# Kernel optimization log

Measured on AMD Instinct MI355X. Metric: run time of the kernel, lower is better.

The kernel has to match this reference:

```python
import jax, jax.numpy as jnp
import numpy as np

NUM_GROUPS = 32
EPS = 1e-6


def group_norm(x, gamma, beta):
    # x: [b, c, h, w]
    b, c, h, w = x.shape
    g = NUM_GROUPS
    xg = x.reshape(b, g, c // g, h, w)
    mean = jnp.mean(xg, axis=(2, 3, 4), keepdims=True)
    var = jnp.var(xg, axis=(2, 3, 4), keepdims=True)
    xg = (xg - mean) * jax.lax.rsqrt(var + EPS)
    x = xg.reshape(b, c, h, w)
    return x * gamma[None, :, None, None] + beta[None, :, None, None]


def conv1x1(x, w, bias):
    # x: [b, c_in, h, w], w: [c_out, c_in], bias: [c_out]
    return jnp.einsum('bihw,oi->bohw', x, w) + bias[None, :, None, None]


def setup_inputs() -> dict:
    key = jax.random.key(0)
    ks = jax.random.split(key, 10)
    c = 512
    b, h, w = 4, 64, 64
    scale = 1.0 / np.sqrt(c)
    inp = {
        'x': jax.random.normal(ks[0], (b, c, h, w), dtype=jnp.float32),
        'gn_gamma': jnp.ones((c,), dtype=jnp.float32),
        'gn_beta': jnp.zeros((c,), dtype=jnp.float32),
        'wq': jax.random.normal(ks[1], (c, c), dtype=jnp.float32) * scale,
        'bq': jnp.zeros((c,), dtype=jnp.float32),
        'wk': jax.random.normal(ks[2], (c, c), dtype=jnp.float32) * scale,
        'bk': jnp.zeros((c,), dtype=jnp.float32),
        'wv': jax.random.normal(ks[3], (c, c), dtype=jnp.float32) * scale,
        'bv': jnp.zeros((c,), dtype=jnp.float32),
        'wo': jax.random.normal(ks[4], (c, c), dtype=jnp.float32) * scale,
        'bo': jnp.zeros((c,), dtype=jnp.float32),
    }
    return inp


def reference(x, gn_gamma, gn_beta, wq, bq, wk, bk, wv, bv, wo, bo):
    b, c, h, w = x.shape
    h_ = group_norm(x, gn_gamma, gn_beta)
    q = conv1x1(h_, wq, bq)
    k = conv1x1(h_, wk, bk)
    v = conv1x1(h_, wv, bv)
    n = h * w
    q = q.reshape(b, c, n).transpose(0, 2, 1)  # [b, n, c]
    k = k.reshape(b, c, n)                      # [b, c, n]
    v = v.reshape(b, c, n).transpose(0, 2, 1)  # [b, n, c]
    sim = jnp.einsum('bqc,bck->bqk', q, k) * (c ** -0.5)  # [b, n, n]
    attn = jax.nn.softmax(sim, axis=-1)
    out = jnp.einsum('bqk,bkc->bqc', attn, v)  # [b, n, c]
    out = out.transpose(0, 2, 1).reshape(b, c, h, w)
    out = conv1x1(out, wo, bo)
    return x + out
```

## Files before the change

kernel.cpp:

```cpp
#include <hip/hip_runtime.h>


typedef __attribute__((ext_vector_type(8))) short bf16x8;
typedef __attribute__((ext_vector_type(4))) float f32x4;

#define MFMA16(a, b, c) __builtin_amdgcn_mfma_f32_16x16x32_bf16((a), (b), (c), 0, 0, 0)

#define B_   4
#define C_   512
#define N_   4096
#define SCALE 0.044194173824159216f
#define ESHIFT 12.0f
#define SC2   0.06376297465050853f
#define ES2   17.312340490667562f

__device__ __forceinline__ unsigned short f2bf(float f) {
    union { float f; unsigned int u; } v; v.f = f;
    unsigned int r = (v.u + 0x7fffu + ((v.u >> 16) & 1u)) >> 16;
    return (unsigned short)r;
}
__device__ __forceinline__ float bf2f(unsigned short s) {
    union { unsigned int u; float f; } v; v.u = ((unsigned int)s) << 16;
    return v.f;
}

__device__ __forceinline__ void async16(const unsigned short* g, unsigned short* l) {
    __builtin_amdgcn_global_load_lds((const __attribute__((address_space(1))) unsigned int*)g,
                                     (__attribute__((address_space(3))) unsigned int*)l,
                                     16, 0, 0);
}

__global__ __launch_bounds__(256) void gn_partial(const float* __restrict__ x,
                                                  float* __restrict__ part) {
    int blk = blockIdx.x;
    int gid = blk >> 2, qtr = blk & 3;
    const float4* base = (const float4*)(x + (size_t)gid * 65536) + qtr * 4096;
    float s = 0.f, ss = 0.f;
    for (int i = threadIdx.x; i < 4096; i += 256) {
        float4 v = base[i];
        s  += v.x + v.y + v.z + v.w;
        ss += v.x * v.x + v.y * v.y + v.z * v.z + v.w * v.w;
    }
    __shared__ float red[512];
    int t = threadIdx.x;
    red[t] = s; red[256 + t] = ss;
    __syncthreads();
    for (int st = 128; st > 0; st >>= 1) {
        if (t < st) { red[t] += red[t + st]; red[256 + t] += red[256 + t + st]; }
        __syncthreads();
    }
    if (t == 0) { part[blk] = red[0]; part[512 + blk] = red[256]; }
}

__global__ __launch_bounds__(256) void gn_apply(const float* __restrict__ x,
                                                const float* __restrict__ gamma,
                                                const float* __restrict__ beta,
                                                const float* __restrict__ part,
                                                unsigned short* __restrict__ ht) {
    __shared__ float tile[64][65];
    __shared__ float mrs[4][2];
    int j0 = blockIdx.x * 64, c0 = blockIdx.y * 64, b = blockIdx.z;
    int t = threadIdx.x;
    if (t < 4) {
        int gid = b * 32 + (c0 >> 4) + t;
        float s = 0.f, ss = 0.f;
#pragma unroll
        for (int q = 0; q < 4; ++q) { s += part[gid * 4 + q]; ss += part[512 + gid * 4 + q]; }
        float mean = s * (1.f / 65536.f);
        float var  = ss * (1.f / 65536.f) - mean * mean;
        mrs[t][0] = mean;
        mrs[t][1] = rsqrtf(var + 1e-6f);
    }
    __syncthreads();
#pragma unroll
    for (int i = 0; i < 16; ++i) {
        int lid = i * 256 + t;
        int cl = lid >> 6, jl = lid & 63;
        int c = c0 + cl;
        float v = x[((size_t)b * C_ + c) * N_ + j0 + jl];
        tile[cl][jl] = (v - mrs[cl >> 4][0]) * mrs[cl >> 4][1] * gamma[c] + beta[c];
    }
    __syncthreads();
#pragma unroll
    for (int i = 0; i < 16; ++i) {
        int lid = i * 256 + t;
        int jl = lid >> 6, cl = lid & 63;
        ht[((size_t)b * N_ + j0 + jl) * C_ + c0 + cl] = f2bf(tile[cl][jl]);
    }
}

__global__ __launch_bounds__(256) void wconv(const float* __restrict__ wq,
                                             const float* __restrict__ wk,
                                             const float* __restrict__ wv,
                                             const float* __restrict__ wo,
                                             unsigned short* __restrict__ dst) {
    size_t i = (size_t)blockIdx.x * 256 + threadIdx.x;
    int m = (int)(i >> 18);
    size_t off = i & 262143;
    const float* src = (m == 0) ? wq : (m == 1) ? wk : (m == 2) ? wv : wo;
    dst[i] = f2bf(src[off]);
}

template <typename EPI>
__device__ __forceinline__ void gemm_core(const unsigned short* __restrict__ Abase,
                                          const unsigned short* __restrict__ Bbase,
                                          size_t lda, size_t ldb, int K, EPI epi) {
    __shared__ unsigned short hl[2][128 * 64];
    __shared__ unsigned short wl[2][128 * 64];
    int t = threadIdx.x;
    int wv = t >> 6, lane = t & 63, l15 = lane & 15, quad = lane >> 4;
    int wm = wv & 1, wn = wv >> 1;
    int srow = lane >> 3;
    int sch  = ((lane & 7) ^ srow) * 8;
    int xr = l15 & 7;
    f32x4 acc[4][4] = {};
#pragma unroll
    for (int i = 0; i < 4; ++i) {
        int seg = wv * 4 + i;
        size_t row = seg * 8 + srow;
        async16(&Abase[row * lda + sch], &hl[0][seg * 512]);
        async16(&Bbase[row * ldb + sch], &wl[0][seg * 512]);
    }
    int nk = K >> 6;
    for (int k = 0; k < nk; ++k) {
        int cur = k & 1;
        __builtin_amdgcn_s_waitcnt(0x3F70);
        __syncthreads();
        if (k + 1 < nk) {
            int k0 = (k + 1) << 6;
#pragma unroll
            for (int i = 0; i < 4; ++i) {
                int seg = wv * 4 + i;
                size_t row = seg * 8 + srow;
                async16(&Abase[row * lda + k0 + sch], &hl[cur ^ 1][seg * 512]);
                async16(&Bbase[row * ldb + k0 + sch], &wl[cur ^ 1][seg * 512]);
            }
        }
#pragma unroll
        for (int kk = 0; kk < 2; ++kk) {
            int sl = (((kk << 2) + quad) ^ xr) * 8;
            bf16x8 af[4], bfr[4];
#pragma unroll
            for (int mi = 0; mi < 4; ++mi)
                af[mi] = *(const bf16x8*)&hl[cur][(wm * 64 + mi * 16 + l15) * 64 + sl];
#pragma unroll
            for (int ni = 0; ni < 4; ++ni)
                bfr[ni] = *(const bf16x8*)&wl[cur][(wn * 64 + ni * 16 + l15) * 64 + sl];
#pragma unroll
            for (int mi = 0; mi < 4; ++mi)
#pragma unroll
                for (int ni = 0; ni < 4; ++ni)
                    acc[mi][ni] = MFMA16(af[mi], bfr[ni], acc[mi][ni]);
        }
    }
    epi(acc, wm, wn, l15, quad);
}

__global__ __launch_bounds__(256) void gemm_qkv(const unsigned short* __restrict__ Ht,
                                                const unsigned short* __restrict__ Wb,
                                                const float* __restrict__ bq,
                                                const float* __restrict__ bk,
                                                const float* __restrict__ bv,
                                                unsigned short* __restrict__ Qt,
                                                unsigned short* __restrict__ Kt,
                                                unsigned short* __restrict__ Vg) {
    int b = blockIdx.z, j0 = blockIdx.x * 128;
    int ct = blockIdx.y;
    int slab = ct >> 2, co0 = (ct & 3) * 128;
    const unsigned short* A = Ht + ((size_t)b * N_ + j0) * C_;
    const unsigned short* B = Wb + (size_t)slab * C_ * C_ + (size_t)co0 * C_;
    const float* bias = (slab == 0) ? bq : (slab == 1) ? bk : bv;
    unsigned short* outqk = (slab == 0) ? Qt : Kt;
    gemm_core(A, B, C_, C_, C_,
        [&](f32x4 (&acc)[4][4], int wm, int wn, int l15, int quad) {
        if (slab < 2) {
#pragma unroll
            for (int mi = 0; mi < 4; ++mi)
#pragma unroll
                for (int ni = 0; ni < 4; ++ni)
#pragma unroll
                    for (int r = 0; r < 4; ++r) {
                        int mrow = wm * 64 + mi * 16 + quad * 4 + r;
                        int ncol = wn * 64 + ni * 16 + l15;
                        outqk[((size_t)b * N_ + j0 + mrow) * C_ + co0 + ncol] =
                            f2bf(acc[mi][ni][r] + bias[co0 + ncol]);
                    }
        } else {
#pragma unroll
            for (int mi = 0; mi < 4; ++mi)
#pragma unroll
                for (int ni = 0; ni < 4; ++ni) {
                    int ncol = wn * 64 + ni * 16 + l15;
                    float bb = bias[co0 + ncol];
                    ushort4 pk;
                    pk.x = f2bf(acc[mi][ni][0] + bb);
                    pk.y = f2bf(acc[mi][ni][1] + bb);
                    pk.z = f2bf(acc[mi][ni][2] + bb);
                    pk.w = f2bf(acc[mi][ni][3] + bb);
                    int jb = j0 + wm * 64 + mi * 16 + quad * 4;
                    *(ushort4*)&Vg[((size_t)b * C_ + co0 + ncol) * N_ + jb] = pk;
                }
        }
    });
}

__global__ __launch_bounds__(512, 2) void gemm_qk_exp(const unsigned short* __restrict__ Qt,
                                                      const unsigned short* __restrict__ Kt,
                                                      unsigned short* __restrict__ P,
                                                      float* __restrict__ psum) {
    extern __shared__ unsigned short sm[];
    int lin = blockIdx.x + 16 * blockIdx.y + 256 * blockIdx.z;
    int xcd = lin & 7;
    int i4  = lin >> 3;
    int idx = i4 & 31;
    int b   = i4 >> 5;
    int rq  = xcd & 3, rk = xcd >> 2;
    int j0  = (rq * 4 + (idx & 3)) * 256;
    int ky  = rk * 8 + (idx >> 2);
    int kc0 = ky * 256;
    const unsigned short* A  = Qt + ((size_t)b * N_ + j0) * C_;
    const unsigned short* Bm = Kt + ((size_t)b * N_ + kc0) * C_;

    int t = threadIdx.x;
    int w = t >> 6, lane = t & 63, l15 = lane & 15, quad = lane >> 4;
    int wm = w >> 2, wn = w & 3;
    int srow = lane >> 2;
    int sch  = (((lane & 3) ^ ((lane >> 3) & 3))) * 8;
    int slotq = (quad ^ ((l15 >> 1) & 3)) * 8;

    f32x4 acc[8][4] = {};

    const int NT = 16;
#pragma unroll
    for (int tt = 0; tt < 2; ++tt) {
        unsigned short* dst = sm + (tt << 14);
        size_t k0 = (size_t)tt << 5;
#pragma unroll
        for (int i = 0; i < 2; ++i) {
            int seg = w * 2 + i;
            size_t row = (size_t)seg * 16 + srow;
            async16(&A [row * C_ + k0 + sch], dst + seg * 512);
            async16(&Bm[row * C_ + k0 + sch], dst + 8192 + seg * 512);
        }
    }
    __builtin_amdgcn_s_waitcnt(0x3F74);
    __builtin_amdgcn_s_barrier();

    for (int tt = 0; tt < NT; tt += 2) {
#pragma unroll
        for (int s = 0; s < 2; ++s) {
            int tc = tt + s;
            const unsigned short* bp = sm + ((tc & 3) << 14);
            int ts = tc + 2;
            unsigned short* stg = sm + ((ts & 3) << 14);
            const bool dostage = (ts < NT);
            size_t k0n = (size_t)ts << 5;
            bf16x8 bfr[4], af[4], af2[4];
#pragma unroll
            for (int ni = 0; ni < 4; ++ni)
                bfr[ni] = *(const bf16x8*)&bp[8192 + (wn * 64 + ni * 16 + l15) * 32 + slotq];
#pragma unroll
            for (int mi = 0; mi < 4; ++mi)
                af[mi] = *(const bf16x8*)&bp[(wm * 128 + mi * 16 + l15) * 32 + slotq];
            if (dostage) {
#pragma unroll
                for (int i = 0; i < 2; ++i) {
                    int seg = w * 2 + i;
                    size_t row = (size_t)seg * 16 + srow;
                    async16(&A[row * C_ + k0n + sch], stg + seg * 512);
                }
            }
            __builtin_amdgcn_s_setprio(1);
#pragma unroll
            for (int mi = 0; mi < 4; ++mi)
#pragma unroll
                for (int ni = 0; ni < 4; ++ni)
                    acc[mi][ni] = MFMA16(af[mi], bfr[ni], acc[mi][ni]);
            __builtin_amdgcn_s_setprio(0);
#pragma unroll
            for (int mi = 0; mi < 4; ++mi)
                af2[mi] = *(const bf16x8*)&bp[(wm * 128 + (mi + 4) * 16 + l15) * 32 + slotq];
            if (dostage) {
#pragma unroll
                for (int i = 0; i < 2; ++i) {
                    int seg = w * 2 + i;
                    size_t row = (size_t)seg * 16 + srow;
                    async16(&Bm[row * C_ + k0n + sch], stg + 8192 + seg * 512);
                }
            }
            __builtin_amdgcn_s_setprio(1);
#pragma unroll
            for (int mi = 0; mi < 4; ++mi)
#pragma unroll
                for (int ni = 0; ni < 4; ++ni)
                    acc[4 + mi][ni] = MFMA16(af2[mi], bfr[ni], acc[4 + mi][ni]);
            __builtin_amdgcn_s_setprio(0);
            if (s == 0) {
                if (tt + 2 < NT) __builtin_amdgcn_s_waitcnt(0x3F74);
                else             __builtin_amdgcn_s_waitcnt(0x3F70);
                __builtin_amdgcn_sched_barrier(0);
            }
        }
        if (tt + 2 < NT) {
            if (tt + 3 < NT) __builtin_amdgcn_s_waitcnt(0x3F74);
            else             __builtin_amdgcn_s_waitcnt(0x3F70);
            __builtin_amdgcn_s_barrier();
        }
    }

#pragma unroll
    for (int mi = 0; mi < 8; ++mi) {
        float rs[4] = {0.f, 0.f, 0.f, 0.f};
#pragma unroll
        for (int ni = 0; ni < 4; ++ni) {
            int ncol = kc0 + wn * 64 + ni * 16 + l15;
#pragma unroll
            for (int r = 0; r < 4; ++r) {
                int mrow = j0 + wm * 128 + mi * 16 + quad * 4 + r;
                float p = exp2f(__builtin_fmaf(acc[mi][ni][r], SC2, -ES2));
                rs[r] += p;
                P[((size_t)b * N_ + mrow) * N_ + ncol] = f2bf(p);
            }
        }
#pragma unroll
        for (int r = 0; r < 4; ++r) {
            float v = rs[r];
            v += __shfl_xor(v, 1);
            v += __shfl_xor(v, 2);
            v += __shfl_xor(v, 4);
            v += __shfl_xor(v, 8);
            if (l15 == 0)
                psum[(size_t)(wn * 16 + ky) * 16384 +
                     (size_t)b * N_ + j0 + wm * 128 + mi * 16 + quad * 4 + r] = v;
        }
    }
}

__global__ __launch_bounds__(512, 2) void gemm_pv(const unsigned short* __restrict__ P,
                                                  const unsigned short* __restrict__ Vg,
                                                  const float* __restrict__ psum,
                                                  unsigned short* __restrict__ ao) {
    extern __shared__ unsigned short sm[];
    __shared__ float linv[256];
    int lin = blockIdx.x;
    int xcd = lin & 7;
    int i4  = lin >> 3;
    int ct  = i4 & 3;
    int grp = xcd + 8 * (i4 >> 2);
    int b = grp & 3, qtile = grp >> 2;
    int j0 = qtile * 256, co0 = ct * 128;
    int t = threadIdx.x;
    int w = t >> 6, lane = t & 63, l15 = lane & 15, quad = lane >> 4;
    int wm = w >> 1, wn = w & 1;
    int srow = lane >> 2;
    int sch  = ((lane & 3) ^ ((lane >> 3) & 3)) * 8;
    int slotq = (quad ^ ((l15 >> 1) & 3)) * 8;
    const unsigned short* A  = P  + ((size_t)b * N_ + j0) * N_;
    const unsigned short* Bm = Vg + ((size_t)b * C_ + co0) * N_;
    f32x4 acc[4][4] = {};
    const int NT = 128;
#pragma unroll
    for (int tt = 0; tt < 2; ++tt) {
        unsigned short* dst = sm + tt * 12288;
        size_t k0 = (size_t)tt << 5;
#pragma unroll
        for (int i = 0; i < 2; ++i) {
            int seg = w * 2 + i;
            size_t row = (size_t)seg * 16 + srow;
            async16(&A[row * N_ + k0 + sch], dst + seg * 512);
        }
        {
            size_t row = (size_t)w * 16 + srow;
            async16(&Bm[row * N_ + k0 + sch], dst + 8192 + w * 512);
        }
    }
    if (t < 256) {
        size_t q = (size_t)b * N_ + j0 + t;
        float s = 0.f;
#pragma unroll
        for (int i = 0; i < 64; ++i) s += psum[(size_t)i * 16384 + q];
        linv[t] = 1.f / s;
    }
    __builtin_amdgcn_s_waitcnt(0x3F73);
    __builtin_amdgcn_s_barrier();
    for (int tt = 0; tt < NT; tt += 2) {
#pragma unroll
        for (int s = 0; s < 2; ++s) {
            int tc = tt + s;
            const unsigned short* bp = sm + (tc & 3) * 12288;
            int ts = tc + 2;
            bf16x8 af[4], bfr[4];
#pragma unroll
            for (int mi = 0; mi < 4; ++mi)
                af[mi] = *(const bf16x8*)&bp[(wm * 64 + mi * 16 + l15) * 32 + slotq];
#pragma unroll
            for (int ni = 0; ni < 4; ++ni)
                bfr[ni] = *(const bf16x8*)&bp[8192 + (wn * 64 + ni * 16 + l15) * 32 + slotq];
            if (ts < NT) {
                unsigned short* stg = sm + (ts & 3) * 12288;
                size_t k0n = (size_t)ts << 5;
#pragma unroll
                for (int i = 0; i < 2; ++i) {
                    int seg = w * 2 + i;
                    size_t row = (size_t)seg * 16 + srow;
                    async16(&A[row * N_ + k0n + sch], stg + seg * 512);
                }
                {
                    size_t row = (size_t)w * 16 + srow;
                    async16(&Bm[row * N_ + k0n + sch], stg + 8192 + w * 512);
                }
            }
            __builtin_amdgcn_s_setprio(1);
#pragma unroll
            for (int mi = 0; mi < 4; ++mi)
#pragma unroll
                for (int ni = 0; ni < 4; ++ni)
                    acc[mi][ni] = MFMA16(af[mi], bfr[ni], acc[mi][ni]);
            __builtin_amdgcn_s_setprio(0);
            if (s == 0) {
                if (tt + 2 < NT) __builtin_amdgcn_s_waitcnt(0x3F73);
                else             __builtin_amdgcn_s_waitcnt(0x3F70);
                __builtin_amdgcn_sched_barrier(0);
            }
        }
        if (tt + 2 < NT) {
            if (tt + 3 < NT) __builtin_amdgcn_s_waitcnt(0x3F73);
            else             __builtin_amdgcn_s_waitcnt(0x3F70);
            __builtin_amdgcn_s_barrier();
        }
    }
#pragma unroll
    for (int mi = 0; mi < 4; ++mi)
#pragma unroll
        for (int ni = 0; ni < 4; ++ni)
#pragma unroll
            for (int r = 0; r < 4; ++r) {
                int mrow = wm * 64 + mi * 16 + quad * 4 + r;
                int ncol = wn * 64 + ni * 16 + l15;
                ao[((size_t)b * N_ + j0 + mrow) * C_ + co0 + ncol] =
                    f2bf(acc[mi][ni][r] * linv[mrow]);
            }
}

__global__ __launch_bounds__(256) void gemm_resid(const unsigned short* __restrict__ AObf,
                                                  const unsigned short* __restrict__ Wo,
                                                  const float* __restrict__ bo,
                                                  const float* __restrict__ xres,
                                                  float* __restrict__ out) {
    int b = blockIdx.z, j0 = blockIdx.x * 128, co0 = blockIdx.y * 128;
    const unsigned short* A = AObf + ((size_t)b * N_ + j0) * C_;
    const unsigned short* B = Wo + (size_t)co0 * C_;
    gemm_core(A, B, C_, C_, C_,
        [&](f32x4 (&acc)[4][4], int wm, int wn, int l15, int quad) {
#pragma unroll
        for (int mi = 0; mi < 4; ++mi)
#pragma unroll
            for (int ni = 0; ni < 4; ++ni) {
                int ncol = wn * 64 + ni * 16 + l15;
                int jb = j0 + wm * 64 + mi * 16 + quad * 4;
                size_t o = ((size_t)b * C_ + co0 + ncol) * N_ + jb;
                float bb = bo[co0 + ncol];
                float4 xr = *(const float4*)&xres[o];
                float4 ov;
                ov.x = acc[mi][ni][0] + bb + xr.x;
                ov.y = acc[mi][ni][1] + bb + xr.y;
                ov.z = acc[mi][ni][2] + bb + xr.z;
                ov.w = acc[mi][ni][3] + bb + xr.w;
                *(float4*)&out[o] = ov;
            }
    });
}

__global__ __launch_bounds__(256, 1) void flash_attn(const unsigned short* __restrict__ Qt,
                                                     const unsigned short* __restrict__ Kt,
                                                     const unsigned short* __restrict__ Vg,
                                                     unsigned short* __restrict__ part,
                                                     float* __restrict__ lbuf,
                                                     int nsplit) {
    extern __shared__ unsigned short smem[];
    unsigned short* Kl = smem;
    unsigned short* Vl = smem + 32768;
    unsigned short* Pl = smem + 65536;

    int flat = blockIdx.x;
    int qblk, b, s;
    if (nsplit == 2) { s = flat & 1; b = (flat >> 1) & 3; qblk = flat >> 3; }
    else             { s = 0;        b = flat & 3;        qblk = flat >> 2; }
    int q0 = qblk * 128;
    int t = threadIdx.x, w = t >> 6, lane = t & 63, l15 = lane & 15, quad = lane >> 4;
    int klen = N_ / nsplit, kbeg = s * klen, nkt = klen / 32;
    int xr = l15 & 7;

    const unsigned short* Kbase = Kt + (size_t)b * N_ * C_;
    const unsigned short* Vbase = Vg + (size_t)b * C_ * N_;

    bf16x8 qa[2][16];
#pragma unroll
    for (int u = 0; u < 2; ++u) {
        const unsigned short* qb =
            Qt + ((size_t)b * N_ + q0 + w * 32 + u * 16 + l15) * C_ + quad * 8;
#pragma unroll
        for (int ck = 0; ck < 16; ++ck) qa[u][ck] = *(const bf16x8*)(qb + ck * 32);
    }

    f32x4 o[2][32] = {};
    float lrow[2][4] = {};

    {
        int k0 = kbeg;
#pragma unroll
        for (int i = 0; i < 8; ++i) {
            int r = w * 8 + i;
            async16(Kbase + (size_t)(k0 + r) * C_ + ((lane ^ (r & 7)) * 8), Kl + r * 512);
        }
#pragma unroll
        for (int i = 0; i < 8; ++i) {
            int idx = w * 8 + i, kc = idx >> 3, cb = idx & 7;
            async16(Vbase + (size_t)(cb * 64 + lane) * N_ + k0 + kc * 8,
                    Vl + (kc * 512 + cb * 64) * 8);
        }
    }

    for (int kt = 0; kt < nkt; ++kt) {
        int cur = kt & 1, nxt = cur ^ 1;
        __builtin_amdgcn_s_waitcnt(0x3F70);
        __syncthreads();
        if (kt + 1 < nkt) {
            int k0 = kbeg + (kt + 1) * 32;
#pragma unroll
            for (int i = 0; i < 8; ++i) {
                int r = w * 8 + i;
                async16(Kbase + (size_t)(k0 + r) * C_ + ((lane ^ (r & 7)) * 8),
                        Kl + nxt * 16384 + r * 512);
            }
#pragma unroll
            for (int i = 0; i < 8; ++i) {
                int idx = w * 8 + i, kc = idx >> 3, cb = idx & 7;
                async16(Vbase + (size_t)(cb * 64 + lane) * N_ + k0 + kc * 8,
                        Vl + nxt * 16384 + (kc * 512 + cb * 64) * 8);
            }
        }
        const unsigned short* Kc = Kl + cur * 16384;
        f32x4 s00 = {}, s01 = {}, s10 = {}, s11 = {};
#pragma unroll
        for (int ck = 0; ck < 16; ++ck) {
            int slot = (ck * 4 + quad) ^ xr;
            bf16x8 b0 = *(const bf16x8*)&Kc[l15 * 512 + slot * 8];
            bf16x8 b1 = *(const bf16x8*)&Kc[(16 + l15) * 512 + slot * 8];
            s00 = MFMA16(qa[0][ck], b0, s00);
            s10 = MFMA16(qa[1][ck], b0, s10);
            s01 = MFMA16(qa[0][ck], b1, s01);
            s11 = MFMA16(qa[1][ck], b1, s11);
        }
        unsigned short* pb = &Pl[w * 1152];
#pragma unroll
        for (int r = 0; r < 4; ++r) {
            float p00 = __expf(s00[r] * SCALE - ESHIFT);
            float p01 = __expf(s01[r] * SCALE - ESHIFT);
            float p10 = __expf(s10[r] * SCALE - ESHIFT);
            float p11 = __expf(s11[r] * SCALE - ESHIFT);
            lrow[0][r] += p00 + p01;
            lrow[1][r] += p10 + p11;
            int row0 = (quad * 4 + r) * 36;
            int row1 = (16 + quad * 4 + r) * 36;
            pb[row0 + l15]      = f2bf(p00);
            pb[row0 + 16 + l15] = f2bf(p01);
            pb[row1 + l15]      = f2bf(p10);
            pb[row1 + 16 + l15] = f2bf(p11);
        }
        __builtin_amdgcn_s_waitcnt(0xC07F);
        bf16x8 pa0 = *(const bf16x8*)&Pl[w * 1152 + l15 * 36 + quad * 8];
        bf16x8 pa1 = *(const bf16x8*)&Pl[w * 1152 + (16 + l15) * 36 + quad * 8];
        const unsigned short* Vc = Vl + cur * 16384;
#pragma unroll
        for (int cf = 0; cf < 32; ++cf) {
            bf16x8 vb = *(const bf16x8*)&Vc[(quad * 512 + cf * 16 + l15) * 8];
            o[0][cf] = MFMA16(pa0, vb, o[0][cf]);
            o[1][cf] = MFMA16(pa1, vb, o[1][cf]);
        }
    }
#pragma unroll
    for (int u = 0; u < 2; ++u)
#pragma unroll
        for (int r = 0; r < 4; ++r) {
            float l = lrow[u][r];
            l += __shfl_xor(l, 1);
            l += __shfl_xor(l, 2);
            l += __shfl_xor(l, 4);
            l += __shfl_xor(l, 8);
            lrow[u][r] = l;
        }
    size_t pbase = (size_t)(s * B_ + b) * N_;
#pragma unroll
    for (int u = 0; u < 2; ++u)
#pragma unroll
        for (int cf = 0; cf < 32; ++cf)
#pragma unroll
            for (int r = 0; r < 4; ++r) {
                int q = q0 + w * 32 + u * 16 + quad * 4 + r;
                part[(pbase + q) * C_ + cf * 16 + l15] = f2bf(o[u][cf][r]);
            }
    if (l15 == 0) {
#pragma unroll
        for (int u = 0; u < 2; ++u)
#pragma unroll
            for (int r = 0; r < 4; ++r) {
                int q = q0 + w * 32 + u * 16 + quad * 4 + r;
                lbuf[pbase + q] = lrow[u][r];
            }
    }
}

__global__ __launch_bounds__(256) void attn_combine(const unsigned short* __restrict__ part,
                                                    const float* __restrict__ lbuf,
                                                    unsigned short* __restrict__ ao,
                                                    int nsplit) {
    size_t idx = (size_t)blockIdx.x * 256 + threadIdx.x;
    int cu = (int)(idx & 63);
    size_t row = idx >> 6;
    float l = lbuf[row];
    union { uint4 v; unsigned short u[8]; } p1, p2, outv;
    p1.v = *(const uint4*)&part[row * C_ + cu * 8];
    if (nsplit == 2) {
        l += lbuf[(size_t)B_ * N_ + row];
        p2.v = *(const uint4*)&part[((size_t)B_ * N_ + row) * C_ + cu * 8];
    } else {
        p2.v = make_uint4(0, 0, 0, 0);
    }
    float inv = 1.f / l;
#pragma unroll
    for (int j = 0; j < 8; ++j)
        outv.u[j] = f2bf((bf2f(p1.u[j]) + bf2f(p2.u[j])) * inv);
    *(uint4*)&ao[row * C_ + cu * 8] = outv.v;
}

extern "C" void kernel_launch(void* const* d_in, const int* in_sizes, int n_in,
                              void* d_out, int out_size, void* d_ws, size_t ws_size,
                              hipStream_t stream) {
    const float* x   = (const float*)d_in[0];
    const float* gam = (const float*)d_in[1];
    const float* bet = (const float*)d_in[2];
    const float* wq  = (const float*)d_in[3];
    const float* bq  = (const float*)d_in[4];
    const float* wk  = (const float*)d_in[5];
    const float* bk  = (const float*)d_in[6];
    const float* wv  = (const float*)d_in[7];
    const float* bv  = (const float*)d_in[8];
    const float* wo  = (const float*)d_in[9];
    const float* bo  = (const float*)d_in[10];
    float* out = (float*)d_out;

    char* ws = (char*)d_ws;
    const size_t SZH = (size_t)B_ * N_ * C_ * 2;
    const size_t OFF_HT = 4096;
    const size_t OFF_QT = OFF_HT + SZH;
    const size_t OFF_KT = OFF_QT + SZH;
    const size_t OFF_VG = OFF_KT + SZH;
    const size_t OFF_WB = OFF_VG + SZH;
    const size_t OFF_X  = OFF_WB + 2097152;
    float*          part0 = (float*)ws;
    unsigned short* Ht    = (unsigned short*)(ws + OFF_HT);
    unsigned short* Qt    = (unsigned short*)(ws + OFF_QT);
    unsigned short* Kt    = (unsigned short*)(ws + OFF_KT);
    unsigned short* Vg    = (unsigned short*)(ws + OFF_VG);
    unsigned short* Wb    = (unsigned short*)(ws + OFF_WB);
    unsigned short* AObf  = Ht;

    const size_t SZPSUM = 64ull * 16384 * 4;
    const size_t SZP    = (size_t)B_ * N_ * N_ * 2;
    float*          psum = (float*)(ws + OFF_X);
    unsigned short* P    = (unsigned short*)(ws + OFF_X + SZPSUM);
    size_t needA = OFF_X + SZPSUM + SZP;

    float*          lbuf = (float*)(ws + OFF_X);
    unsigned short* partb = (unsigned short*)(ws + OFF_X + 262144);
    size_t needB2 = OFF_X + 262144 + 2 * SZH;

    gn_partial<<<512, 256, 0, stream>>>(x, part0);
    gn_apply<<<dim3(64, 8, B_), 256, 0, stream>>>(x, gam, bet, part0, Ht);
    wconv<<<4096, 256, 0, stream>>>(wq, wk, wv, wo, Wb);
    gemm_qkv<<<dim3(32, 12, B_), 256, 0, stream>>>(Ht, Wb, bq, bk, bv, Qt, Kt, Vg);

    if (ws_size >= needA) {
        const int QK_LDS = 131072;
        (void)hipFuncSetAttribute((const void*)gemm_qk_exp,
                                  hipFuncAttributeMaxDynamicSharedMemorySize, QK_LDS);
        gemm_qk_exp<<<dim3(16, 16, B_), 512, QK_LDS, stream>>>(Qt, Kt, P, psum);
        const int PV_LDS = 98304;
        (void)hipFuncSetAttribute((const void*)gemm_pv,
                                  hipFuncAttributeMaxDynamicSharedMemorySize, PV_LDS);
        gemm_pv<<<256, 512, PV_LDS, stream>>>(P, Vg, psum, AObf);
    } else {
        int nsplit = (ws_size >= needB2) ? 2 : 1;
        const int FLASH_LDS = 140288;
        (void)hipFuncSetAttribute((const void*)flash_attn,
                                  hipFuncAttributeMaxDynamicSharedMemorySize, FLASH_LDS);
        flash_attn<<<dim3(32 * B_ * nsplit), 256, FLASH_LDS, stream>>>(Qt, Kt, Vg, partb, lbuf, nsplit);
        attn_combine<<<4096, 256, 0, stream>>>(partb, lbuf, AObf, nsplit);
    }
    gemm_resid<<<dim3(32, 4, B_), 256, 0, stream>>>(AObf, Wb + 786432, bo, x, out);
}
```

Measured before the change: 320.7 us.

## Shrink QK-exp tile to 256x128 with triple-buffered LDS and higher occupancy

Cuts the QK^T+exp GEMM tile from 256x256 to 256x128 and gives each wave a 64x64 sub-tile, which halves the accumulator registers. The grid becomes a 2048-block 1D launch with a new XCD-aware swizzle. The LDS pipeline moves from a four-stage ring with two sub-steps per iteration to a rotating three-buffer scheme of 24 KB each, so 73 KB per block, and launch bounds rise to allow four blocks per CU. The aim is better latency hiding through occupancy, at the cost of less operand reuse per tile and more global K/Q traffic. The psum layout is reindexed to match the new column split.

```diff
diff --git a/kernel.cpp b/kernel.cpp
--- a/kernel.cpp
+++ b/kernel.cpp
@@ -204,119 +204,91 @@
     });
 }
 
-__global__ __launch_bounds__(512, 2) void gemm_qk_exp(const unsigned short* __restrict__ Qt,
+__global__ __launch_bounds__(512, 4) void gemm_qk_exp(const unsigned short* __restrict__ Qt,
                                                       const unsigned short* __restrict__ Kt,
                                                       unsigned short* __restrict__ P,
                                                       float* __restrict__ psum) {
     extern __shared__ unsigned short sm[];
-    int lin = blockIdx.x + 16 * blockIdx.y + 256 * blockIdx.z;
+    int lin = blockIdx.x;
     int xcd = lin & 7;
-    int i4  = lin >> 3;
-    int idx = i4 & 31;
-    int b   = i4 >> 5;
-    int rq  = xcd & 3, rk = xcd >> 2;
-    int j0  = (rq * 4 + (idx & 3)) * 256;
-    int ky  = rk * 8 + (idx >> 2);
-    int kc0 = ky * 256;
+    int i   = lin >> 3;
+    int rid = xcd + 8 * (i >> 4);
+    int idx = i & 15;
+    int mi4 = idx & 1, ni4 = idx >> 1;
+    int b   = rid >> 5;
+    int rem = rid & 31;
+    int rm  = rem & 7, rn = rem >> 3;
+    int j0  = (rm * 2 + mi4) * 256;
+    int ky  = rn * 8 + ni4;
+    int kc0 = ky * 128;
     const unsigned short* A  = Qt + ((size_t)b * N_ + j0) * C_;
     const unsigned short* Bm = Kt + ((size_t)b * N_ + kc0) * C_;
 
     int t = threadIdx.x;
     int w = t >> 6, lane = t & 63, l15 = lane & 15, quad = lane >> 4;
-    int wm = w >> 2, wn = w & 3;
+    int wm = w >> 1, wn = w & 1;
     int srow = lane >> 2;
-    int sch  = (((lane & 3) ^ ((lane >> 3) & 3))) * 8;
+    int sch  = ((lane & 3) ^ ((lane >> 3) & 3)) * 8;
     int slotq = (quad ^ ((l15 >> 1) & 3)) * 8;
 
-    f32x4 acc[8][4] = {};
-
+    const unsigned short* gA0 = A + ((size_t)(w * 2 + 0) * 16 + srow) * C_ + sch;
+    const unsigned short* gA1 = A + ((size_t)(w * 2 + 1) * 16 + srow) * C_ + sch;
+    const unsigned short* gB  = Bm + ((size_t)w * 16 + srow) * C_ + sch;
+
+    f32x4 acc[4][4] = {};
     const int NT = 16;
-#pragma unroll
-    for (int tt = 0; tt < 2; ++tt) {
-        unsigned short* dst = sm + (tt << 14);
-        size_t k0 = (size_t)tt << 5;
-#pragma unroll
-        for (int i = 0; i < 2; ++i) {
-            int seg = w * 2 + i;
-            size_t row = (size_t)seg * 16 + srow;
-            async16(&A [row * C_ + k0 + sch], dst + seg * 512);
-            async16(&Bm[row * C_ + k0 + sch], dst + 8192 + seg * 512);
-        }
-    }
-    __builtin_amdgcn_s_waitcnt(0x3F74);
+    unsigned short* bA = sm;
+    unsigned short* bB = sm + 12288;
+    unsigned short* bC = sm + 24576;
+
+    async16(gA0,      bA + (w * 2 + 0) * 512);
+    async16(gA1,      bA + (w * 2 + 1) * 512);
+    async16(gB,       bA + 8192 + w * 512);
+    async16(gA0 + 32, bB + (w * 2 + 0) * 512);
+    async16(gA1 + 32, bB + (w * 2 + 1) * 512);
+    async16(gB  + 32, bB + 8192 + w * 512);
+    gA0 += 64; gA1 += 64; gB += 64;
+    __builtin_amdgcn_s_waitcnt(0x3F73);
     __builtin_amdgcn_s_barrier();
 
-    for (int tt = 0; tt < NT; tt += 2) {
-#pragma unroll
-        for (int s = 0; s < 2; ++s) {
-            int tc = tt + s;
-            const unsigned short* bp = sm + ((tc & 3) << 14);
-            int ts = tc + 2;
-            unsigned short* stg = sm + ((ts & 3) << 14);
-            const bool dostage = (ts < NT);
-            size_t k0n = (size_t)ts << 5;
-            bf16x8 bfr[4], af[4], af2[4];
+    for (int tt = 0; tt < NT; ++tt) {
+        if (tt + 2 < NT) {
+            async16(gA0, bC + (w * 2 + 0) * 512);
+            async16(gA1, bC + (w * 2 + 1) * 512);
+            async16(gB,  bC + 8192 + w * 512);
+            gA0 += 32; gA1 += 32; gB += 32;
+        }
+        bf16x8 af[4], bfr[4];
+#pragma unroll
+        for (int mi = 0; mi < 4; ++mi)
+            af[mi] = *(const bf16x8*)&bA[(wm * 64 + mi * 16 + l15) * 32 + slotq];
+#pragma unroll
+        for (int ni = 0; ni < 4; ++ni)
+            bfr[ni] = *(const bf16x8*)&bA[8192 + (wn * 64 + ni * 16 + l15) * 32 + slotq];
+        __builtin_amdgcn_s_setprio(1);
+#pragma unroll
+        for (int mi = 0; mi < 4; ++mi)
 #pragma unroll
             for (int ni = 0; ni < 4; ++ni)
-                bfr[ni] = *(const bf16x8*)&bp[8192 + (wn * 64 + ni * 16 + l15) * 32 + slotq];
-#pragma unroll
-            for (int mi = 0; mi < 4; ++mi)
-                af[mi] = *(const bf16x8*)&bp[(wm * 128 + mi * 16 + l15) * 32 + slotq];
-            if (dostage) {
-#pragma unroll
-                for (int i = 0; i < 2; ++i) {
-                    int seg = w * 2 + i;
-                    size_t row = (size_t)seg * 16 + srow;
-                    async16(&A[row * C_ + k0n + sch], stg + seg * 512);
-                }
-            }
-            __builtin_amdgcn_s_setprio(1);
-#pragma unroll
-            for (int mi = 0; mi < 4; ++mi)
-#pragma unroll
-                for (int ni = 0; ni < 4; ++ni)
-                    acc[mi][ni] = MFMA16(af[mi], bfr[ni], acc[mi][ni]);
-            __builtin_amdgcn_s_setprio(0);
-#pragma unroll
-            for (int mi = 0; mi < 4; ++mi)
-                af2[mi] = *(const bf16x8*)&bp[(wm * 128 + (mi + 4) * 16 + l15) * 32 + slotq];
-            if (dostage) {
-#pragma unroll
-                for (int i = 0; i < 2; ++i) {
-                    int seg = w * 2 + i;
-                    size_t row = (size_t)seg * 16 + srow;
-                    async16(&Bm[row * C_ + k0n + sch], stg + 8192 + seg * 512);
-                }
-            }
-            __builtin_amdgcn_s_setprio(1);
-#pragma unroll
-            for (int mi = 0; mi < 4; ++mi)
-#pragma unroll
-                for (int ni = 0; ni < 4; ++ni)
-                    acc[4 + mi][ni] = MFMA16(af2[mi], bfr[ni], acc[4 + mi][ni]);
-            __builtin_amdgcn_s_setprio(0);
-            if (s == 0) {
-                if (tt + 2 < NT) __builtin_amdgcn_s_waitcnt(0x3F74);
-                else             __builtin_amdgcn_s_waitcnt(0x3F70);
-                __builtin_amdgcn_sched_barrier(0);
-            }
-        }
-        if (tt + 2 < NT) {
-            if (tt + 3 < NT) __builtin_amdgcn_s_waitcnt(0x3F74);
+                acc[mi][ni] = MFMA16(af[mi], bfr[ni], acc[mi][ni]);
+        __builtin_amdgcn_s_setprio(0);
+        if (tt + 1 < NT) {
+            if (tt + 2 < NT) __builtin_amdgcn_s_waitcnt(0x3F73);
             else             __builtin_amdgcn_s_waitcnt(0x3F70);
             __builtin_amdgcn_s_barrier();
         }
-    }
-
-#pragma unroll
-    for (int mi = 0; mi < 8; ++mi) {
+        unsigned short* tmp = bA; bA = bB; bB = bC; bC = tmp;
+    }
+
+#pragma unroll
+    for (int mi = 0; mi < 4; ++mi) {
         float rs[4] = {0.f, 0.f, 0.f, 0.f};
 #pragma unroll
         for (int ni = 0; ni < 4; ++ni) {
             int ncol = kc0 + wn * 64 + ni * 16 + l15;
 #pragma unroll
             for (int r = 0; r < 4; ++r) {
-                int mrow = j0 + wm * 128 + mi * 16 + quad * 4 + r;
+                int mrow = j0 + wm * 64 + mi * 16 + quad * 4 + r;
                 float p = exp2f(__builtin_fmaf(acc[mi][ni][r], SC2, -ES2));
                 rs[r] += p;
                 P[((size_t)b * N_ + mrow) * N_ + ncol] = f2bf(p);
@@ -330,8 +302,8 @@
             v += __shfl_xor(v, 4);
             v += __shfl_xor(v, 8);
             if (l15 == 0)
-                psum[(size_t)(wn * 16 + ky) * 16384 +
-                     (size_t)b * N_ + j0 + wm * 128 + mi * 16 + quad * 4 + r] = v;
+                psum[(size_t)(ky * 2 + wn) * 16384 +
+                     (size_t)b * N_ + j0 + wm * 64 + mi * 16 + quad * 4 + r] = v;
         }
     }
 }
@@ -682,10 +654,10 @@
     gemm_qkv<<<dim3(32, 12, B_), 256, 0, stream>>>(Ht, Wb, bq, bk, bv, Qt, Kt, Vg);
 
     if (ws_size >= needA) {
-        const int QK_LDS = 131072;
+        const int QK_LDS = 73728;
         (void)hipFuncSetAttribute((const void*)gemm_qk_exp,
                                   hipFuncAttributeMaxDynamicSharedMemorySize, QK_LDS);
-        gemm_qk_exp<<<dim3(16, 16, B_), 512, QK_LDS, stream>>>(Qt, Kt, P, psum);
+        gemm_qk_exp<<<2048, 512, QK_LDS, stream>>>(Qt, Kt, P, psum);
         const int PV_LDS = 98304;
         (void)hipFuncSetAttribute((const void*)gemm_pv,
                                   hipFuncAttributeMaxDynamicSharedMemorySize, PV_LDS);
```

New measurement: 320.2 us. Within noise of the previous version (-0.2%).
